# Kernel tuning notes

Hardware: AMD Instinct MI355X
Metric: run time of the kernel (lower is better)

Reference implementation:

```python
import jax, jax.numpy as jnp
import numpy as np
from jax import lax

B, N, D, HF, WF = 2, 4, 256, 32, 32
P = 30000
IMG_W, IMG_H = 512, 512
GX, GY, GZ = 60, 60, 8
HO, WO = HF * 8, WF * 8  # deconv upsamples x8
EPS = 1e-5


def setup_inputs():
    key = jax.random.key(0)
    ks = jax.random.split(key, 8)
    clip_vision = jax.random.normal(ks[0], (B, N, D, HF, WF), jnp.float32)
    pixel_coordinates = jax.random.uniform(ks[1], (B, N, P, 2), jnp.float32) * jnp.array([IMG_W - 1.0, IMG_H - 1.0], jnp.float32)
    v0 = jax.random.randint(ks[2], (B, P, 1), 0, GX)
    v1 = jax.random.randint(ks[3], (B, P, 1), 0, GY)
    v2 = jax.random.randint(ks[4], (B, P, 1), 0, GZ)
    pol_voxel_ind = jnp.concatenate([v0, v1, v2], axis=-1).astype(jnp.int32)
    w1 = jax.random.normal(ks[5], (64, D, 7, 7), jnp.float32) * np.float32(np.sqrt(2.0 / (D * 49)))
    w2 = jax.random.normal(ks[6], (64, 64, 7, 7), jnp.float32) * np.float32(np.sqrt(2.0 / (64 * 49)))
    w3 = jax.random.normal(ks[7], (D, 64, 3, 3), jnp.float32) * np.float32(np.sqrt(2.0 / (64 * 9)))
    gamma = jnp.ones((D,), jnp.float32)
    beta = jnp.zeros((D,), jnp.float32)
    return dict(clip_vision=clip_vision, pixel_coordinates=pixel_coordinates,
                pol_voxel_ind=pol_voxel_ind, w1=w1, w2=w2, w3=w3, gamma=gamma, beta=beta)


def _conv(x, w, pad):
    return lax.conv_general_dilated(x, w, (1, 1), [(pad, pad), (pad, pad)],
                                    dimension_numbers=('NCHW', 'OIHW', 'NCHW'))


def _up_nearest2x(x):
    return jnp.repeat(jnp.repeat(x, 2, axis=2), 2, axis=3)


def _up_bilinear2x_ac(x):
    # torch UpsamplingBilinear2d -> align_corners=True
    _, _, H, W = x.shape
    def idx_w(n_in, n_out):
        pos = jnp.arange(n_out, dtype=x.dtype) * ((n_in - 1) / (n_out - 1))
        i0 = jnp.floor(pos).astype(jnp.int32)
        i1 = jnp.minimum(i0 + 1, n_in - 1)
        return i0, i1, (pos - i0).astype(x.dtype)
    i0, i1, wy = idx_w(H, 2 * H)
    x = x[:, :, i0, :] * (1 - wy)[None, None, :, None] + x[:, :, i1, :] * wy[None, None, :, None]
    j0, j1, wx = idx_w(W, 2 * W)
    x = x[:, :, :, j0] * (1 - wx) + x[:, :, :, j1] * wx
    return x


def _deconv(x, w1, w2, w3):
    x = jax.nn.relu(_conv(x, w1, 3))
    x = _up_nearest2x(x)
    x = jax.nn.relu(_conv(x, w2, 3))
    x = _up_nearest2x(x)
    x = jax.nn.relu(_conv(x, w3, 1))
    return _up_bilinear2x_ac(x)


def reference(clip_vision, pixel_coordinates, pol_voxel_ind, w1, w2, w3, gamma, beta):
    fmap = _deconv(clip_vision.reshape(B * N, D, HF, WF), w1, w2, w3).reshape(B, N, D, HO, WO)
    fm = fmap.reshape(B, N, D, HO * WO)

    # faithful reproduction of the source normalization (y uses already-normalized x)
    gx = pixel_coordinates[..., 0] / (IMG_W * 0.5) - 1.0
    gy = gx / (IMG_H * 0.5) - 1.0
    # grid_sample bilinear, align_corners=False, zero padding
    ix = ((gx + 1.0) * WO - 1.0) * 0.5
    iy = ((gy + 1.0) * HO - 1.0) * 0.5
    x0f = jnp.floor(ix); y0f = jnp.floor(iy)
    x0 = x0f.astype(jnp.int32); y0 = y0f.astype(jnp.int32)
    wx1 = ix - x0f; wy1 = iy - y0f

    def corner(yi, xi, w):  # [B,N,P] idx -> [B,N,D,P] weighted vals
        valid = (yi >= 0) & (yi < HO) & (xi >= 0) & (xi < WO)
        yc = jnp.clip(yi, 0, HO - 1); xc = jnp.clip(xi, 0, WO - 1)
        idx = (yc * WO + xc)[:, :, None, :]
        vals = jnp.take_along_axis(fm, idx, axis=3)
        return vals * (w * valid)[:, :, None, :]

    sampled = (corner(y0, x0, (1 - wy1) * (1 - wx1)) +
               corner(y0, x0 + 1, (1 - wy1) * wx1) +
               corner(y0 + 1, x0, wy1 * (1 - wx1)) +
               corner(y0 + 1, x0 + 1, wy1 * wx1))  # [B,N,D,P]

    # faithful reproduction of `.view(-1, D)` on [1,D,P,1]: row-major reshape
    pts = sampled.reshape(B, N, P, D)
    feats = pts.mean(axis=1).reshape(B * P, D)

    # BatchNorm1d (training mode: biased batch stats)
    mu = feats.mean(axis=0)
    var = jnp.mean((feats - mu) ** 2, axis=0)
    feats = (feats - mu) * lax.rsqrt(var + EPS) * gamma + beta

    # DynamicScatter mean-reduce over (batch, voxel) keys -> dense per-voxel means
    b_idx = jnp.arange(B, dtype=jnp.int32)[:, None]
    lin = (((b_idx * GX + pol_voxel_ind[..., 0]) * GY + pol_voxel_ind[..., 1]) * GZ + pol_voxel_ind[..., 2]).reshape(-1)
    nseg = B * GX * GY * GZ
    sums = jax.ops.segment_sum(feats, lin, num_segments=nseg)
    cnt = jax.ops.segment_sum(jnp.ones((B * P,), feats.dtype), lin, num_segments=nseg)
    voxel_feats = sums / jnp.maximum(cnt, 1.0)[:, None]

    allv = jnp.arange(nseg, dtype=jnp.int32)
    bb = allv // (GX * GY * GZ); r = allv % (GX * GY * GZ)
    voxel_coors = jnp.stack([bb, r // (GY * GZ), (r % (GY * GZ)) // GZ, r % GZ], axis=1)
    return voxel_feats, voxel_coors
```

## Files before the change

kernel.cpp:

```cpp
#include <hip/hip_runtime.h>

#define NB   2
#define NN   4
#define ND   256
#define NP   30000
#define NSEG 57600
#define NROWS 60000
#define DG   8
#define CAP  16

static const size_t OFF_SBF   = 0;
static const size_t OFF_C1P   = 0;
static const size_t OFF_C2P   = 2000000ull;
static const size_t OFF_C3P   = 4000000ull;
static const size_t OFF_C1    = 7680000ull;
static const size_t OFF_C2    = OFF_C1  + 32768ull;
static const size_t OFF_C3    = OFF_C2  + 32768ull;
static const size_t OFF_FM    = OFF_C3  + 262144ull;
static const size_t OFF_PTAB  = OFF_FM  + 524288ull;
static const size_t OFF_CNTI  = OFF_PTAB + 960000ull;
static const size_t OFF_IDX2  = OFF_CNTI + 57600ull;
static const size_t OFF_SCALE = OFF_IDX2 + 921600ull;
static const size_t OFF_SHIFT = OFF_SCALE + 256ull;
static const size_t OFF_SUM   = OFF_SHIFT + 256ull;
static const size_t OFF_SUMSQ = OFF_SUM + 512ull;

__device__ __forceinline__ unsigned short f2bf(float f) {
    unsigned u = __float_as_uint(f);
    u = u + 0x7FFFu + ((u >> 16) & 1u);
    return (unsigned short)(u >> 16);
}
__device__ __forceinline__ float bf2f(unsigned short h) {
    return __uint_as_float(((unsigned)h) << 16);
}

__global__ void conv1_partial_k(const float* __restrict__ in, const float* __restrict__ w1,
                                float* __restrict__ part) {
    __shared__ float in_s[8][8][40];
    __shared__ float w_s[8][8][49];
    int bx = blockIdx.x;
    int s   = bx >> 6;
    int r6  = bx & 63;
    int img = r6 >> 3;
    int oc0 = (r6 & 7) * 8;
    int tid = threadIdx.x;

    for (int idx = tid; idx < 2560; idx += 256) {
        int col = idx % 40;
        int row = (idx / 40) & 7;
        int ic  = idx / 320;
        float v = 0.f;
        if (row >= 3 && col >= 3 && col < 35)
            v = in[((size_t)(img * 256 + s * 8 + ic) * 32 + (row - 3)) * 32 + (col - 3)];
        in_s[ic][row][col] = v;
    }
    for (int idx = tid; idx < 3136; idx += 256) {
        int ocl = idx / 392;
        int rem = idx % 392;
        int ic  = rem / 49;
        int k   = rem % 49;
        w_s[ocl][ic][k] = w1[((size_t)(oc0 + ocl) * 256 + s * 8 + ic) * 49 + k];
    }
    __syncthreads();

    int c  = tid & 31;
    int r  = (tid >> 5) & 1;
    int ol = tid >> 6;
    float a0 = 0.f, a1 = 0.f;
    for (int ic = 0; ic < 8; ++ic) {
        const float* wA = &w_s[ol][ic][0];
        const float* wB = &w_s[ol + 4][ic][0];
#pragma unroll
        for (int kr = 0; kr < 7; ++kr) {
            const float* ip = &in_s[ic][r + kr][c];
#pragma unroll
            for (int kc = 0; kc < 7; ++kc) {
                float iv = ip[kc];
                a0 += iv * wA[kr * 7 + kc];
                a1 += iv * wB[kr * 7 + kc];
            }
        }
    }
    size_t base = (size_t)s * 32768 + img * 4096 + (oc0 + ol) * 64 + r * 32 + c;
    part[base]       = a0;
    part[base + 256] = a1;
}

__global__ void conv1_reduce_k(const float* __restrict__ part, float* __restrict__ conv1) {
    int o = blockIdx.x * blockDim.x + threadIdx.x;
    float a = 0.f;
#pragma unroll
    for (int s = 0; s < 32; ++s) a += part[(size_t)s * 32768 + o];
    conv1[o] = fmaxf(a, 0.f);
}

__global__ void conv2_partial_k(const float* __restrict__ conv1, const float* __restrict__ w2,
                                float* __restrict__ part) {
    __shared__ float up_s[8][4][72];
    __shared__ float w_s2[4][8][49];
    int bx = blockIdx.x;
    int s   = bx >> 7;
    int r7  = bx & 127;
    int img = r7 >> 4;
    int oc0 = (r7 & 15) * 4;
    int tid = threadIdx.x;

    for (int idx = tid; idx < 2304; idx += 256) {
        int col = idx % 72;
        int ur  = (idx / 72) & 3;
        int ic  = idx / 288;
        float v = 0.f;
        if (col >= 3 && col < 67)
            v = conv1[(size_t)(img * 64 + s * 8 + ic) * 64 + (ur >> 1) * 32 + ((col - 3) >> 1)];
        up_s[ic][ur][col] = v;
    }
    for (int idx = tid; idx < 1568; idx += 256) {
        int ocl = idx / 392;
        int rem = idx % 392;
        int ic  = rem / 49;
        int k   = rem % 49;
        w_s2[ocl][ic][k] = w2[((size_t)(oc0 + ocl) * 64 + s * 8 + ic) * 49 + k];
    }
    __syncthreads();

    int c2 = tid & 63;
    int ol = tid >> 6;
    float acc = 0.f;
    for (int ic = 0; ic < 8; ++ic) {
#pragma unroll
        for (int ur = 0; ur < 4; ++ur) {
            const float* ip = &up_s[ic][ur][c2];
            const float* wr = &w_s2[ol][ic][(ur + 3) * 7];
#pragma unroll
            for (int kc = 0; kc < 7; ++kc) acc += ip[kc] * wr[kc];
        }
    }
    part[(size_t)s * 32768 + img * 4096 + (oc0 + ol) * 64 + c2] = acc;
}

__global__ void conv2_reduce_k(const float* __restrict__ part, float* __restrict__ conv2) {
    int o = blockIdx.x * blockDim.x + threadIdx.x;
    float a = 0.f;
#pragma unroll
    for (int s = 0; s < 8; ++s) a += part[(size_t)s * 32768 + o];
    conv2[o] = fmaxf(a, 0.f);
}

__global__ void conv3_partial_k(const float* __restrict__ conv2, const float* __restrict__ w3,
                                float* __restrict__ part) {
    __shared__ float row_s[16][132];
    __shared__ float wc_s[2][16][4];
    int bx = blockIdx.x;
    int s    = bx >> 10;
    int r10  = bx & 1023;
    int img  = r10 >> 7;
    int oc0  = (r10 & 127) * 2;
    int tid  = threadIdx.x;

    for (int idx = tid; idx < 2112; idx += 256) {
        int col = idx % 132;
        int ic  = idx / 132;
        float v = 0.f;
        if (col >= 1 && col < 129)
            v = conv2[(size_t)(img * 64 + s * 16 + ic) * 64 + ((col - 1) >> 1)];
        row_s[ic][col] = v;
    }
    if (tid < 96) {
        int ocl = tid / 48;
        int ic  = (tid / 3) % 16;
        int kc  = tid % 3;
        const float* wp = w3 + ((size_t)(oc0 + ocl) * 64 + s * 16 + ic) * 9;
        wc_s[ocl][ic][kc] = wp[3 + kc] + wp[6 + kc];
    }
    __syncthreads();

    int c3 = tid & 127;
    int ol = tid >> 7;
    float acc = 0.f;
    for (int ic = 0; ic < 16; ++ic) {
        const float* ip = &row_s[ic][c3];
#pragma unroll
        for (int kc = 0; kc < 3; ++kc) acc += ip[kc] * wc_s[ol][ic][kc];
    }
    part[(size_t)s * 262144 + img * 32768 + (oc0 + ol) * 128 + c3] = acc;
}

__global__ void conv3_reduce_k(const float* __restrict__ part, float* __restrict__ conv3) {
    int o = blockIdx.x * blockDim.x + threadIdx.x;
    float a = part[o] + part[262144 + o] + part[524288 + o] + part[786432 + o];
    conv3[o] = fmaxf(a, 0.f);
}

__global__ void bilin_k(const float* __restrict__ conv3, float* __restrict__ fm) {
    int o = blockIdx.x * blockDim.x + threadIdx.x;
    int x = o & 255;
    int rest = o >> 8;
    const float f = (float)(127.0 / 255.0);
    float pos = (float)x * f;
    float i0f = floorf(pos);
    int i0 = (int)i0f;
    int i1 = min(i0 + 1, 127);
    float w = pos - i0f;
    const float* rp = conv3 + (size_t)rest * 128;
    fm[o] = rp[i0] * (1.f - w) + rp[i1] * w;
}

__global__ void pixtab_k(const float* __restrict__ pix, float* __restrict__ ptab) {
    int t = blockIdx.x * 256 + threadIdx.x;
    if (t >= NB * NN * NP) return;
    float px = pix[(size_t)t * 2];
    float gx = px / 256.0f - 1.0f;
    float gy = gx / 256.0f - 1.0f;
    float ix = ((gx + 1.0f) * 256.0f - 1.0f) * 0.5f;
    float iy = ((gy + 1.0f) * 256.0f - 1.0f) * 0.5f;
    float x0f = floorf(ix), y0f = floorf(iy);
    int x0 = (int)x0f, y0 = (int)y0f;
    float wx1 = ix - x0f, wy1 = iy - y0f;
    float wrow = 0.f;
    if (y0 == 0) wrow += 1.0f - wy1;
    if (y0 + 1 == 0) wrow += wy1;
    wrow *= 0.25f;
    bool ok0 = (x0 >= 0) && (x0 < 256);
    int x1 = x0 + 1;
    bool ok1 = (x1 >= 0) && (x1 < 256);
    float4 v;
    v.x = ok0 ? wrow * (1.0f - wx1) : 0.f;
    v.y = ok1 ? wrow * wx1 : 0.f;
    v.z = __int_as_float(min(max(x0, 0), 255));
    v.w = __int_as_float(min(max(x1, 0), 255));
    ((float4*)ptab)[t] = v;
}

__global__ void listbuild_k(const int* __restrict__ vox, unsigned* __restrict__ cntI,
                            unsigned* __restrict__ idx2) {
    int r = blockIdx.x * 256 + threadIdx.x;
    if (r >= NROWS) return;
    int v0 = vox[3 * r], v1 = vox[3 * r + 1], v2 = vox[3 * r + 2];
    int b = (r >= NP) ? 1 : 0;
    int lin = ((b * 60 + v0) * 60 + v1) * 8 + v2;
    unsigned slot = atomicAdd(&cntI[lin], 1u);
    if (slot < CAP) idx2[(size_t)lin * CAP + slot] = (unsigned)r;
}

__global__ void sample_k(const float* __restrict__ fm, const float* __restrict__ ptab,
                         unsigned short* __restrict__ Sbf, double* __restrict__ sum,
                         double* __restrict__ sumsq) {
    __shared__ __align__(16) unsigned short rows_bf[4][256][DG];
    __shared__ float bsum[256], bsq[256];
    int bx = blockIdx.x;
    int b  = bx >> 5;
    int d0 = (bx & 31) * DG;
    int tid = threadIdx.x;

#pragma unroll
    for (int i = 0; i < 32; ++i) {
        int dd = i & 7;
        int n  = i >> 3;
        rows_bf[n][tid][dd] = f2bf(fm[((size_t)((b * 4 + n) * 256 + d0 + dd)) * 256 + tid]);
    }
    bsum[tid] = 0.f;
    bsq[tid]  = 0.f;
    __syncthreads();

    const int CHUNK = 1000;
    int p0 = blockIdx.y * CHUNK;
    float lsum[DG], lsq[DG];
#pragma unroll
    for (int dd = 0; dd < DG; ++dd) { lsum[dd] = 0.f; lsq[dd] = 0.f; }

    const float4* pt = (const float4*)ptab + (size_t)(b * 4) * NP;
    unsigned short* Sb = Sbf + (size_t)b * (ND * NP);

    for (int p = p0 + tid; p < p0 + CHUNK; p += 256) {
        float acc[DG];
#pragma unroll
        for (int dd = 0; dd < DG; ++dd) acc[dd] = 0.f;
#pragma unroll
        for (int n = 0; n < 4; ++n) {
            float4 tv = pt[(size_t)n * NP + p];
            float ws0 = tv.x, ws1 = tv.y;
            int x0c = __float_as_int(tv.z);
            int x1c = __float_as_int(tv.w);
            uint4 q0 = *(const uint4*)&rows_bf[n][x0c][0];
            uint4 q1 = *(const uint4*)&rows_bf[n][x1c][0];
#define ACC2(j, w0r, w1r)                                                        \
            acc[2*(j)]   += ws0 * __uint_as_float((w0r) << 16)                    \
                          + ws1 * __uint_as_float((w1r) << 16);                   \
            acc[2*(j)+1] += ws0 * __uint_as_float((w0r) & 0xFFFF0000u)            \
                          + ws1 * __uint_as_float((w1r) & 0xFFFF0000u);
            ACC2(0, q0.x, q1.x)
            ACC2(1, q0.y, q1.y)
            ACC2(2, q0.z, q1.z)
            ACC2(3, q0.w, q1.w)
#undef ACC2
        }
#pragma unroll
        for (int dd = 0; dd < DG; ++dd) {
            float a = acc[dd];
            Sb[(size_t)(d0 + dd) * NP + p] = f2bf(a);
            lsum[dd] += a;
            lsq[dd]  += a * a;
        }
    }
#pragma unroll
    for (int dd = 0; dd < DG; ++dd) {
        int cc = (48 * (d0 + dd) + p0 + tid) & 255;
        atomicAdd(&bsum[cc], lsum[dd]);
        atomicAdd(&bsq[cc], lsq[dd]);
    }
    __syncthreads();
    atomicAdd(&sum[tid], (double)bsum[tid]);
    atomicAdd(&sumsq[tid], (double)bsq[tid]);
}

__global__ void scaleshift_k(const double* __restrict__ sum, const double* __restrict__ sumsq,
                             const float* __restrict__ gamma, const float* __restrict__ beta,
                             float* __restrict__ scale, float* __restrict__ shift) {
    int d = threadIdx.x;
    double mu = sum[d] / 60000.0;
    double var = sumsq[d] / 60000.0 - mu * mu;
    float rs = 1.0f / sqrtf((float)var + 1e-5f);
    float sc = rs * gamma[d];
    scale[d] = sc;
    shift[d] = beta[d] - (float)mu * sc;
}

__global__ void gather_k(const unsigned short* __restrict__ Sbf,
                         const unsigned* __restrict__ cntI, const unsigned* __restrict__ idx2,
                         const float* __restrict__ scale, const float* __restrict__ shift,
                         float* __restrict__ out, float* __restrict__ coors) {
    int v = blockIdx.x;
    int tid = threadIdx.x;
    unsigned k = cntI[v];
    unsigned kk = (k < CAP) ? k : CAP;
    float acc = 0.f;
    for (unsigned i = 0; i < kk; ++i) {
        unsigned r = idx2[(size_t)v * CAP + i];
        acc += bf2f(Sbf[(size_t)r * 256 + tid]);
    }
    float val = 0.f;
    if (k) val = fmaf(acc / (float)k, scale[tid], shift[tid]);
    out[(size_t)v * 256 + tid] = val;
    if (tid < 4) {
        int bb = v / 28800, rr = v % 28800;
        int x = (tid == 0) ? bb : (tid == 1) ? rr / 480 : (tid == 2) ? (rr % 480) / 8 : rr % 8;
        coors[(size_t)v * 4 + tid] = (float)x;
    }
}

extern "C" void kernel_launch(void* const* d_in, const int* in_sizes, int n_in,
                              void* d_out, int out_size, void* d_ws, size_t ws_size,
                              hipStream_t stream) {
    const float* clip  = (const float*)d_in[0];
    const float* pix   = (const float*)d_in[1];
    const int*   vox   = (const int*)d_in[2];
    const float* w1    = (const float*)d_in[3];
    const float* w2    = (const float*)d_in[4];
    const float* w3    = (const float*)d_in[5];
    const float* gamma = (const float*)d_in[6];
    const float* beta  = (const float*)d_in[7];
    float* out = (float*)d_out;
    float* ws  = (float*)d_ws;

    unsigned short* Sbf = (unsigned short*)(ws + OFF_SBF);
    float*    c1p   = ws + OFF_C1P;
    float*    c2p   = ws + OFF_C2P;
    float*    c3p   = ws + OFF_C3P;
    float*    c1    = ws + OFF_C1;
    float*    c2    = ws + OFF_C2;
    float*    c3    = ws + OFF_C3;
    float*    fm    = ws + OFF_FM;
    float*    ptab  = ws + OFF_PTAB;
    unsigned* cntI  = (unsigned*)(ws + OFF_CNTI);
    unsigned* idx2  = (unsigned*)(ws + OFF_IDX2);
    float*    scale = ws + OFF_SCALE;
    float*    shift = ws + OFF_SHIFT;
    double*   sum   = (double*)(ws + OFF_SUM);
    double*   sumsq = (double*)(ws + OFF_SUMSQ);

    hipMemsetAsync((void*)cntI, 0, NSEG * sizeof(unsigned), stream);
    hipMemsetAsync((void*)sum, 0, 2 * 256 * sizeof(double), stream);

    conv1_partial_k<<<2048, 256, 0, stream>>>(clip, w1, c1p);
    conv1_reduce_k<<<128, 256, 0, stream>>>(c1p, c1);
    conv2_partial_k<<<1024, 256, 0, stream>>>(c1, w2, c2p);
    conv2_reduce_k<<<128, 256, 0, stream>>>(c2p, c2);
    conv3_partial_k<<<4096, 256, 0, stream>>>(c2, w3, c3p);
    conv3_reduce_k<<<1024, 256, 0, stream>>>(c3p, c3);
    bilin_k<<<2048, 256, 0, stream>>>(c3, fm);
    pixtab_k<<<(NB * NN * NP + 255) / 256, 256, 0, stream>>>(pix, ptab);
    listbuild_k<<<(NROWS + 255) / 256, 256, 0, stream>>>(vox, cntI, idx2);
    sample_k<<<dim3(64, 30), 256, 0, stream>>>(fm, ptab, Sbf, sum, sumsq);
    scaleshift_k<<<1, 256, 0, stream>>>(sum, sumsq, gamma, beta, scale, shift);
    gather_k<<<NSEG, 256, 0, stream>>>(Sbf, cntI, idx2, scale, shift,
                                       out, out + (size_t)NSEG * 256);
}
```

Measured before the change: 272.0 us.

## Fuse bilinear upsample into sampler, merge aux kernels, vectorize sampling and gather

The bilinear upsample now runs inside sample_k's shared-memory load, which drops the fm buffer and one launch. The pixel-table and voxel-list kernels are merged into one launch, and the two memsets are merged into one by making the workspace regions contiguous. sample_k handles two points per thread and writes packed bf16 pairs. gather_k handles two voxels per block with paired bf16 loads and float2 stores. The aim is to cut launch count, extra global traffic and scalar memory ops, at the cost of more registers in sample_k under launch bounds.

```diff
diff --git a/kernel.cpp b/kernel.cpp
--- a/kernel.cpp
+++ b/kernel.cpp
@@ -16,14 +16,13 @@
 static const size_t OFF_C1    = 7680000ull;
 static const size_t OFF_C2    = OFF_C1  + 32768ull;
 static const size_t OFF_C3    = OFF_C2  + 32768ull;
-static const size_t OFF_FM    = OFF_C3  + 262144ull;
-static const size_t OFF_PTAB  = OFF_FM  + 524288ull;
+static const size_t OFF_PTAB  = OFF_C3  + 262144ull;
 static const size_t OFF_CNTI  = OFF_PTAB + 960000ull;
-static const size_t OFF_IDX2  = OFF_CNTI + 57600ull;
-static const size_t OFF_SCALE = OFF_IDX2 + 921600ull;
+static const size_t OFF_SUM   = OFF_CNTI + 57600ull;
+static const size_t OFF_SUMSQ = OFF_SUM  + 512ull;
+static const size_t OFF_SCALE = OFF_SUMSQ + 512ull;
 static const size_t OFF_SHIFT = OFF_SCALE + 256ull;
-static const size_t OFF_SUM   = OFF_SHIFT + 256ull;
-static const size_t OFF_SUMSQ = OFF_SUM + 512ull;
+static const size_t OFF_IDX2  = OFF_SHIFT + 256ull;
 
 __device__ __forceinline__ unsigned short f2bf(float f) {
     unsigned u = __float_as_uint(f);
@@ -191,60 +190,46 @@
     conv3[o] = fmaxf(a, 0.f);
 }
 
-__global__ void bilin_k(const float* __restrict__ conv3, float* __restrict__ fm) {
-    int o = blockIdx.x * blockDim.x + threadIdx.x;
-    int x = o & 255;
-    int rest = o >> 8;
-    const float f = (float)(127.0 / 255.0);
-    float pos = (float)x * f;
-    float i0f = floorf(pos);
-    int i0 = (int)i0f;
-    int i1 = min(i0 + 1, 127);
-    float w = pos - i0f;
-    const float* rp = conv3 + (size_t)rest * 128;
-    fm[o] = rp[i0] * (1.f - w) + rp[i1] * w;
-}
-
-__global__ void pixtab_k(const float* __restrict__ pix, float* __restrict__ ptab) {
+__global__ void aux_k(const float* __restrict__ pix, float* __restrict__ ptab,
+                      const int* __restrict__ vox, unsigned* __restrict__ cntI,
+                      unsigned* __restrict__ idx2) {
     int t = blockIdx.x * 256 + threadIdx.x;
-    if (t >= NB * NN * NP) return;
-    float px = pix[(size_t)t * 2];
-    float gx = px / 256.0f - 1.0f;
-    float gy = gx / 256.0f - 1.0f;
-    float ix = ((gx + 1.0f) * 256.0f - 1.0f) * 0.5f;
-    float iy = ((gy + 1.0f) * 256.0f - 1.0f) * 0.5f;
-    float x0f = floorf(ix), y0f = floorf(iy);
-    int x0 = (int)x0f, y0 = (int)y0f;
-    float wx1 = ix - x0f, wy1 = iy - y0f;
-    float wrow = 0.f;
-    if (y0 == 0) wrow += 1.0f - wy1;
-    if (y0 + 1 == 0) wrow += wy1;
-    wrow *= 0.25f;
-    bool ok0 = (x0 >= 0) && (x0 < 256);
-    int x1 = x0 + 1;
-    bool ok1 = (x1 >= 0) && (x1 < 256);
-    float4 v;
-    v.x = ok0 ? wrow * (1.0f - wx1) : 0.f;
-    v.y = ok1 ? wrow * wx1 : 0.f;
-    v.z = __int_as_float(min(max(x0, 0), 255));
-    v.w = __int_as_float(min(max(x1, 0), 255));
-    ((float4*)ptab)[t] = v;
-}
-
-__global__ void listbuild_k(const int* __restrict__ vox, unsigned* __restrict__ cntI,
-                            unsigned* __restrict__ idx2) {
-    int r = blockIdx.x * 256 + threadIdx.x;
-    if (r >= NROWS) return;
-    int v0 = vox[3 * r], v1 = vox[3 * r + 1], v2 = vox[3 * r + 2];
-    int b = (r >= NP) ? 1 : 0;
-    int lin = ((b * 60 + v0) * 60 + v1) * 8 + v2;
-    unsigned slot = atomicAdd(&cntI[lin], 1u);
-    if (slot < CAP) idx2[(size_t)lin * CAP + slot] = (unsigned)r;
-}
-
-__global__ void sample_k(const float* __restrict__ fm, const float* __restrict__ ptab,
-                         unsigned short* __restrict__ Sbf, double* __restrict__ sum,
-                         double* __restrict__ sumsq) {
+    if (t < NB * NN * NP) {
+        float px = pix[(size_t)t * 2];
+        float gx = px / 256.0f - 1.0f;
+        float gy = gx / 256.0f - 1.0f;
+        float ix = ((gx + 1.0f) * 256.0f - 1.0f) * 0.5f;
+        float iy = ((gy + 1.0f) * 256.0f - 1.0f) * 0.5f;
+        float x0f = floorf(ix), y0f = floorf(iy);
+        int x0 = (int)x0f, y0 = (int)y0f;
+        float wx1 = ix - x0f, wy1 = iy - y0f;
+        float wrow = 0.f;
+        if (y0 == 0) wrow += 1.0f - wy1;
+        if (y0 + 1 == 0) wrow += wy1;
+        wrow *= 0.25f;
+        bool ok0 = (x0 >= 0) && (x0 < 256);
+        int x1 = x0 + 1;
+        bool ok1 = (x1 >= 0) && (x1 < 256);
+        float4 v;
+        v.x = ok0 ? wrow * (1.0f - wx1) : 0.f;
+        v.y = ok1 ? wrow * wx1 : 0.f;
+        v.z = __int_as_float(min(max(x0, 0), 255));
+        v.w = __int_as_float(min(max(x1, 0), 255));
+        ((float4*)ptab)[t] = v;
+    }
+    if (t < NROWS) {
+        int v0 = vox[3 * t], v1 = vox[3 * t + 1], v2 = vox[3 * t + 2];
+        int b = (t >= NP) ? 1 : 0;
+        int lin = ((b * 60 + v0) * 60 + v1) * 8 + v2;
+        unsigned slot = atomicAdd(&cntI[lin], 1u);
+        if (slot < CAP) idx2[(size_t)lin * CAP + slot] = (unsigned)t;
+    }
+}
+
+__global__ void __launch_bounds__(256, 4)
+sample_k(const float* __restrict__ conv3, const float* __restrict__ ptab,
+         unsigned short* __restrict__ Sbf, double* __restrict__ sum,
+         double* __restrict__ sumsq) {
     __shared__ __align__(16) unsigned short rows_bf[4][256][DG];
     __shared__ float bsum[256], bsq[256];
     int bx = blockIdx.x;
@@ -252,11 +237,20 @@
     int d0 = (bx & 31) * DG;
     int tid = threadIdx.x;
 
-#pragma unroll
-    for (int i = 0; i < 32; ++i) {
-        int dd = i & 7;
-        int n  = i >> 3;
-        rows_bf[n][tid][dd] = f2bf(fm[((size_t)((b * 4 + n) * 256 + d0 + dd)) * 256 + tid]);
+    {
+        const float f = (float)(127.0 / 255.0);
+        float pos = (float)tid * f;
+        float i0f = floorf(pos);
+        int i0 = (int)i0f;
+        int i1 = min(i0 + 1, 127);
+        float w = pos - i0f;
+#pragma unroll
+        for (int i = 0; i < 32; ++i) {
+            int dd = i & 7;
+            int n  = i >> 3;
+            const float* rp = conv3 + (size_t)((b * 4 + n) * 256 + d0 + dd) * 128;
+            rows_bf[n][tid][dd] = f2bf(rp[i0] * (1.f - w) + rp[i1] * w);
+        }
     }
     bsum[tid] = 0.f;
     bsq[tid]  = 0.f;
@@ -264,49 +258,58 @@
 
     const int CHUNK = 1000;
     int p0 = blockIdx.y * CHUNK;
-    float lsum[DG], lsq[DG];
-#pragma unroll
-    for (int dd = 0; dd < DG; ++dd) { lsum[dd] = 0.f; lsq[dd] = 0.f; }
+    float lsA[DG], lqA[DG], lsB[DG], lqB[DG];
+#pragma unroll
+    for (int dd = 0; dd < DG; ++dd) { lsA[dd] = lqA[dd] = lsB[dd] = lqB[dd] = 0.f; }
 
     const float4* pt = (const float4*)ptab + (size_t)(b * 4) * NP;
     unsigned short* Sb = Sbf + (size_t)b * (ND * NP);
 
-    for (int p = p0 + tid; p < p0 + CHUNK; p += 256) {
-        float acc[DG];
-#pragma unroll
-        for (int dd = 0; dd < DG; ++dd) acc[dd] = 0.f;
+    for (int pA = p0 + 2 * tid; pA < p0 + CHUNK; pA += 512) {
+        int pB = pA + 1;
+        float accA[DG], accB[DG];
+#pragma unroll
+        for (int dd = 0; dd < DG; ++dd) { accA[dd] = 0.f; accB[dd] = 0.f; }
 #pragma unroll
         for (int n = 0; n < 4; ++n) {
-            float4 tv = pt[(size_t)n * NP + p];
-            float ws0 = tv.x, ws1 = tv.y;
-            int x0c = __float_as_int(tv.z);
-            int x1c = __float_as_int(tv.w);
-            uint4 q0 = *(const uint4*)&rows_bf[n][x0c][0];
-            uint4 q1 = *(const uint4*)&rows_bf[n][x1c][0];
-#define ACC2(j, w0r, w1r)                                                        \
-            acc[2*(j)]   += ws0 * __uint_as_float((w0r) << 16)                    \
-                          + ws1 * __uint_as_float((w1r) << 16);                   \
-            acc[2*(j)+1] += ws0 * __uint_as_float((w0r) & 0xFFFF0000u)            \
-                          + ws1 * __uint_as_float((w1r) & 0xFFFF0000u);
-            ACC2(0, q0.x, q1.x)
-            ACC2(1, q0.y, q1.y)
-            ACC2(2, q0.z, q1.z)
-            ACC2(3, q0.w, q1.w)
+            float4 tA = pt[(size_t)n * NP + pA];
+            float4 tB = pt[(size_t)n * NP + pB];
+            uint4 a0 = *(const uint4*)&rows_bf[n][__float_as_int(tA.z)][0];
+            uint4 a1 = *(const uint4*)&rows_bf[n][__float_as_int(tA.w)][0];
+            uint4 b0 = *(const uint4*)&rows_bf[n][__float_as_int(tB.z)][0];
+            uint4 b1 = *(const uint4*)&rows_bf[n][__float_as_int(tB.w)][0];
+#define ACC2(dst, j, w0, w1, q0, q1)                                             \
+            dst[2*(j)]   += (w0) * __uint_as_float((q0) << 16)                    \
+                          + (w1) * __uint_as_float((q1) << 16);                   \
+            dst[2*(j)+1] += (w0) * __uint_as_float((q0) & 0xFFFF0000u)            \
+                          + (w1) * __uint_as_float((q1) & 0xFFFF0000u);
+            ACC2(accA, 0, tA.x, tA.y, a0.x, a1.x)
+            ACC2(accA, 1, tA.x, tA.y, a0.y, a1.y)
+            ACC2(accA, 2, tA.x, tA.y, a0.z, a1.z)
+            ACC2(accA, 3, tA.x, tA.y, a0.w, a1.w)
+            ACC2(accB, 0, tB.x, tB.y, b0.x, b1.x)
+            ACC2(accB, 1, tB.x, tB.y, b0.y, b1.y)
+            ACC2(accB, 2, tB.x, tB.y, b0.z, b1.z)
+            ACC2(accB, 3, tB.x, tB.y, b0.w, b1.w)
 #undef ACC2
         }
 #pragma unroll
         for (int dd = 0; dd < DG; ++dd) {
-            float a = acc[dd];
-            Sb[(size_t)(d0 + dd) * NP + p] = f2bf(a);
-            lsum[dd] += a;
-            lsq[dd]  += a * a;
+            float aA = accA[dd], aB = accB[dd];
+            unsigned pk = (unsigned)f2bf(aA) | ((unsigned)f2bf(aB) << 16);
+            *(unsigned*)&Sb[(size_t)(d0 + dd) * NP + pA] = pk;
+            lsA[dd] += aA; lqA[dd] += aA * aA;
+            lsB[dd] += aB; lqB[dd] += aB * aB;
         }
     }
 #pragma unroll
     for (int dd = 0; dd < DG; ++dd) {
-        int cc = (48 * (d0 + dd) + p0 + tid) & 255;
-        atomicAdd(&bsum[cc], lsum[dd]);
-        atomicAdd(&bsq[cc], lsq[dd]);
+        int ccA = (48 * (d0 + dd) + p0 + 2 * tid) & 255;
+        int ccB = (ccA + 1) & 255;
+        atomicAdd(&bsum[ccA], lsA[dd]);
+        atomicAdd(&bsq[ccA],  lqA[dd]);
+        atomicAdd(&bsum[ccB], lsB[dd]);
+        atomicAdd(&bsq[ccB],  lqB[dd]);
     }
     __syncthreads();
     atomicAdd(&sum[tid], (double)bsum[tid]);
@@ -329,22 +332,30 @@
                          const unsigned* __restrict__ cntI, const unsigned* __restrict__ idx2,
                          const float* __restrict__ scale, const float* __restrict__ shift,
                          float* __restrict__ out, float* __restrict__ coors) {
-    int v = blockIdx.x;
-    int tid = threadIdx.x;
+    int v = blockIdx.x * 2 + (threadIdx.x >> 7);
+    int lane = threadIdx.x & 127;
     unsigned k = cntI[v];
     unsigned kk = (k < CAP) ? k : CAP;
-    float acc = 0.f;
+    float a0 = 0.f, a1 = 0.f;
     for (unsigned i = 0; i < kk; ++i) {
         unsigned r = idx2[(size_t)v * CAP + i];
-        acc += bf2f(Sbf[(size_t)r * 256 + tid]);
-    }
-    float val = 0.f;
-    if (k) val = fmaf(acc / (float)k, scale[tid], shift[tid]);
-    out[(size_t)v * 256 + tid] = val;
-    if (tid < 4) {
+        unsigned pr = *(const unsigned*)&Sbf[(size_t)r * 256 + lane * 2];
+        a0 += __uint_as_float(pr << 16);
+        a1 += __uint_as_float(pr & 0xFFFF0000u);
+    }
+    float2 st;
+    if (k) {
+        float inv = 1.0f / (float)k;
+        st.x = fmaf(a0 * inv, scale[lane * 2],     shift[lane * 2]);
+        st.y = fmaf(a1 * inv, scale[lane * 2 + 1], shift[lane * 2 + 1]);
+    } else {
+        st.x = 0.f; st.y = 0.f;
+    }
+    *(float2*)&out[(size_t)v * 256 + lane * 2] = st;
+    if (lane < 4) {
         int bb = v / 28800, rr = v % 28800;
-        int x = (tid == 0) ? bb : (tid == 1) ? rr / 480 : (tid == 2) ? (rr % 480) / 8 : rr % 8;
-        coors[(size_t)v * 4 + tid] = (float)x;
+        int x = (lane == 0) ? bb : (lane == 1) ? rr / 480 : (lane == 2) ? (rr % 480) / 8 : rr % 8;
+        coors[(size_t)v * 4 + lane] = (float)x;
     }
 }
 
@@ -369,17 +380,15 @@
     float*    c1    = ws + OFF_C1;
     float*    c2    = ws + OFF_C2;
     float*    c3    = ws + OFF_C3;
-    float*    fm    = ws + OFF_FM;
     float*    ptab  = ws + OFF_PTAB;
     unsigned* cntI  = (unsigned*)(ws + OFF_CNTI);
-    unsigned* idx2  = (unsigned*)(ws + OFF_IDX2);
+    double*   sum   = (double*)(ws + OFF_SUM);
+    double*   sumsq = (double*)(ws + OFF_SUMSQ);
     float*    scale = ws + OFF_SCALE;
     float*    shift = ws + OFF_SHIFT;
-    double*   sum   = (double*)(ws + OFF_SUM);
-    double*   sumsq = (double*)(ws + OFF_SUMSQ);
-
-    hipMemsetAsync((void*)cntI, 0, NSEG * sizeof(unsigned), stream);
-    hipMemsetAsync((void*)sum, 0, 2 * 256 * sizeof(double), stream);
+    unsigned* idx2  = (unsigned*)(ws + OFF_IDX2);
+
+    hipMemsetAsync((void*)cntI, 0, NSEG * sizeof(unsigned) + 1024 * sizeof(float), stream);
 
     conv1_partial_k<<<2048, 256, 0, stream>>>(clip, w1, c1p);
     conv1_reduce_k<<<128, 256, 0, stream>>>(c1p, c1);
@@ -387,11 +396,9 @@
     conv2_reduce_k<<<128, 256, 0, stream>>>(c2p, c2);
     conv3_partial_k<<<4096, 256, 0, stream>>>(c2, w3, c3p);
     conv3_reduce_k<<<1024, 256, 0, stream>>>(c3p, c3);
-    bilin_k<<<2048, 256, 0, stream>>>(c3, fm);
-    pixtab_k<<<(NB * NN * NP + 255) / 256, 256, 0, stream>>>(pix, ptab);
-    listbuild_k<<<(NROWS + 255) / 256, 256, 0, stream>>>(vox, cntI, idx2);
-    sample_k<<<dim3(64, 30), 256, 0, stream>>>(fm, ptab, Sbf, sum, sumsq);
+    aux_k<<<(NB * NN * NP + 255) / 256, 256, 0, stream>>>(pix, ptab, vox, cntI, idx2);
+    sample_k<<<dim3(64, 30), 256, 0, stream>>>(c3, ptab, Sbf, sum, sumsq);
     scaleshift_k<<<1, 256, 0, stream>>>(sum, sumsq, gamma, beta, scale, shift);
-    gather_k<<<NSEG, 256, 0, stream>>>(Sbf, cntI, idx2, scale, shift,
-                                       out, out + (size_t)NSEG * 256);
-}
+    gather_k<<<NSEG / 2, 256, 0, stream>>>(Sbf, cntI, idx2, scale, shift,
+                                           out, out + (size_t)NSEG * 256);
+}
```

New measurement: 307.1 us. +12.9%, slower.
